# Kernel tuning notes

Hardware: AMD Instinct MI355X
Metric: run time of the kernel (lower is better)

## Reference

```python
import jax, jax.numpy as jnp
import numpy as np

H = 32          # num_heads
DN = 128        # qk_nope_head_dim
DR = 64         # qk_rope_head_dim
DV = 128        # v_head_dim
HID = 4096      # hidden_size
QR = 1536       # q_lora_rank
KVR = 512       # kv_lora_rank
EPS = 1e-6
MAXP = 4096     # max_position_embeddings


def _rope_tables():
    inv_freq = 1.0 / (10000.0 ** (np.arange(0, DR, 2, dtype=np.float32) / DR))
    t = np.arange(MAXP, dtype=np.float32)
    freqs = np.outer(t, inv_freq)
    emb = np.concatenate([freqs, freqs], axis=-1)  # [MAXP, DR]
    return jnp.asarray(np.cos(emb), jnp.float32), jnp.asarray(np.sin(emb), jnp.float32)


def _rotate_half(x):
    x1, x2 = x[..., : x.shape[-1] // 2], x[..., x.shape[-1] // 2 :]
    return jnp.concatenate([-x2, x1], axis=-1)


def _rms_norm(x, w, eps=EPS):
    var = jnp.mean(jnp.square(x), axis=-1, keepdims=True)
    return x * jax.lax.rsqrt(var + eps) * w


def setup_inputs() -> dict:
    key = jax.random.key(0)
    ks = jax.random.split(key, 9)
    s = 0.02
    return {
        "hidden_states": jax.random.normal(ks[0], (2, 2048, HID), jnp.float32),
        "position_ids": jnp.arange(2 * 2048, dtype=jnp.int64).reshape(2, 2048) % MAXP,
        "q_a_w": jax.random.normal(ks[1], (QR, HID), jnp.float32) * s,
        "q_a_ln_w": jnp.ones((QR,), jnp.float32),
        "q_b_w": jax.random.normal(ks[2], (H * (DN + DR), QR), jnp.float32) * s,
        "kv_a_w": jax.random.normal(ks[3], (KVR, HID), jnp.float32) * s,
        "kv_a_ln_w": jnp.ones((KVR,), jnp.float32),
        "kv_b_w": jax.random.normal(ks[4], (H * (DN + DV), KVR), jnp.float32) * s,
        "k_rope_w": jax.random.normal(ks[5], (H * DR, HID), jnp.float32) * s,
        "o_w": jax.random.normal(ks[6], (HID, H * DV), jnp.float32) * s,
    }


def reference(hidden_states, position_ids, q_a_w, q_a_ln_w, q_b_w,
              kv_a_w, kv_a_ln_w, kv_b_w, k_rope_w, o_w):
    bsz, q_len, _ = hidden_states.shape
    cos_tab, sin_tab = _rope_tables()

    # Q low-rank path
    q = hidden_states @ q_a_w.T                      # [B,S,QR]
    q = _rms_norm(q, q_a_ln_w)
    q = q @ q_b_w.T                                  # [B,S,H*(DN+DR)]
    q = q.reshape(bsz, q_len, H, DN + DR).transpose(0, 2, 1, 3)  # [B,H,S,DN+DR]
    q_nope, q_rope = q[..., :DN], q[..., DN:]

    # KV low-rank path
    kv = _rms_norm(hidden_states @ kv_a_w.T, kv_a_ln_w)          # [B,S,KVR]
    kv = (kv @ kv_b_w.T).reshape(bsz, q_len, H, DN + DV).transpose(0, 2, 1, 3)
    k_nope, v = kv[..., :DN], kv[..., DN:]                        # [B,H,S,DN],[B,H,S,DV]

    k_rope = (hidden_states @ k_rope_w.T).reshape(bsz, q_len, H, DR).transpose(0, 2, 1, 3)

    # decoupled RoPE
    cos = cos_tab[position_ids][:, None, :, :]       # [B,1,S,DR]
    sin = sin_tab[position_ids][:, None, :, :]
    q_rope = q_rope * cos + _rotate_half(q_rope) * sin
    k_rope = k_rope * cos + _rotate_half(k_rope) * sin

    full_q = jnp.concatenate([q_nope, q_rope], axis=-1)  # [B,H,S,DN+DR]
    full_k = jnp.concatenate([k_nope, k_rope], axis=-1)

    scale = 1.0 / jnp.sqrt(jnp.float32(DN + DR))
    attn = jnp.einsum("bhqd,bhkd->bhqk", full_q, full_k) * scale
    attn = jax.nn.softmax(attn.astype(jnp.float32), axis=-1).astype(full_q.dtype)
    out = jnp.einsum("bhqk,bhkd->bhqd", attn, v)          # [B,H,S,DV]
    out = out.transpose(0, 2, 1, 3).reshape(bsz, q_len, H * DV)
    return out @ o_w.T                                     # [B,S,HID]
```

## Files before the change

### kernel.cpp

```cpp
#include <hip/hip_runtime.h>
#include <hip/hip_bf16.h>
#include <math.h>


typedef __attribute__((ext_vector_type(8))) short s16x8;
typedef __attribute__((ext_vector_type(4))) float f32x4;
typedef __attribute__((ext_vector_type(4))) unsigned short u16x4;

#define DEV __device__ __forceinline__

constexpr int Bc = 2, Sc = 2048, Tc = Bc * Sc;
constexpr int Hc = 32, DNc = 128, DRc = 64, DVc = 128;
constexpr int HIDc = 4096, QRc = 1536, KVRc = 512;
constexpr int DQK = DNc + DRc;

DEV unsigned short f2bf(float f) {
  unsigned u = __float_as_uint(f);
  return (unsigned short)((u + 0x7fffu + ((u >> 16) & 1u)) >> 16);
}
DEV float bf2f(unsigned short u) { return __uint_as_float(((unsigned)u) << 16); }

DEV void gll16(const void* g, void* l) {
  __builtin_amdgcn_global_load_lds((const __attribute__((address_space(1))) void*)g,
                                   (__attribute__((address_space(3))) void*)l, 16, 0, 0);
}
DEV f32x4 mfma_bf16(s16x8 a, s16x8 b, f32x4 c) {
  return __builtin_amdgcn_mfma_f32_16x16x32_bf16(a, b, c, 0, 0, 0);
}
DEV unsigned cvt_pk_bf16(float a, float b) {
  unsigned r;
  asm("v_cvt_pk_bf16_f32 %0, %1, %2" : "=v"(r) : "v"(a), "v"(b));
  return r;
}

__global__ __launch_bounds__(256) void cast_k(const float* __restrict__ in,
                                              unsigned short* __restrict__ out, long n) {
  long i = ((long)blockIdx.x * 256 + threadIdx.x) * 4;
  if (i >= n) return;
  float4 v = *(const float4*)(in + i);
  u16x4 o;
  o.x = f2bf(v.x); o.y = f2bf(v.y); o.z = f2bf(v.z); o.w = f2bf(v.w);
  *(u16x4*)(out + i) = o;
}

template <int COLS>
__global__ __launch_bounds__(256) void rmsnorm_bf_k(unsigned short* __restrict__ x,
                                                    const float* __restrict__ w,
                                                    int pitch) {
  const int row = blockIdx.x;
  unsigned short* p = x + (size_t)row * pitch;
  float ss = 0.f;
  for (int c = threadIdx.x * 8; c < COLS; c += 2048) {
    s16x8 v = *(const s16x8*)&p[c];
    #pragma unroll
    for (int j = 0; j < 8; ++j) { const float f = bf2f((unsigned short)v[j]); ss += f * f; }
  }
  #pragma unroll
  for (int off = 1; off < 64; off <<= 1) ss += __shfl_xor(ss, off, 64);
  __shared__ float sred[4];
  if ((threadIdx.x & 63) == 0) sred[threadIdx.x >> 6] = ss;
  __syncthreads();
  const float inv = rsqrtf((sred[0] + sred[1] + sred[2] + sred[3]) / (float)COLS + 1e-6f);
  for (int c = threadIdx.x * 8; c < COLS; c += 2048) {
    s16x8 v = *(const s16x8*)&p[c];
    s16x8 o;
    #pragma unroll
    for (int j = 0; j < 8; ++j)
      o[j] = (short)f2bf(bf2f((unsigned short)v[j]) * inv * w[c + j]);
    *(s16x8*)&p[c] = o;
  }
}

template <int MODE>
__global__ __launch_bounds__(512, 2) void gemm256_bt(const unsigned short* __restrict__ A,
                                                     int lda,
                                                     const unsigned short* __restrict__ B,
                                                     void* __restrict__ Cout,
                                                     void* __restrict__ Cout2,
                                                     int M, int N, int K) {
  __shared__ unsigned short As[2][256 * 64];
  __shared__ unsigned short Bs[2][256 * 64];
  const int tid = threadIdx.x;
  const int wv = tid >> 6, l = tid & 63;
  const int lo = l & 15, hi = l >> 4;
  const int wm = wv >> 2, wn = wv & 3;
  const int nbx = N >> 8;
  const int nwg = (M >> 8) * nbx;
  const int orig = blockIdx.x;
  const int q8 = nwg >> 3, r8 = nwg & 7, xc = orig & 7, o8 = orig >> 3;
  const int wg = (xc < r8 ? xc * (q8 + 1) : r8 * (q8 + 1) + (xc - r8) * q8) + o8;
  const int bx = wg % nbx, by = wg / nbx;
  const int m0 = by * 256, n0 = bx * 256;
  const int lrow = l >> 3;
  const int lcol = (((l & 7) ^ lrow) << 3);

  f32x4 acc[8][4] = {};
  const int NKT = K >> 6;

  auto stage = [&](int bi, int kt) {
    #pragma unroll
    for (int i = 0; i < 4; ++i) {
      const int r0 = wv * 32 + i * 8;
      gll16(A + (size_t)(m0 + r0 + lrow) * lda + kt + lcol, (void*)&As[bi][r0 * 64]);
    }
    #pragma unroll
    for (int i = 0; i < 4; ++i) {
      const int r0 = wv * 32 + i * 8;
      gll16(B + (size_t)(n0 + r0 + lrow) * K + kt + lcol, (void*)&Bs[bi][r0 * 64]);
    }
  };

  stage(0, 0);

  for (int t = 0; t < NKT; ++t) {
    const int bi = t & 1;
    if (t + 1 < NKT) stage(bi ^ 1, (t + 1) * 64);
    __builtin_amdgcn_sched_barrier(0);
    if (t + 1 < NKT) asm volatile("s_waitcnt vmcnt(8)" ::: "memory");
    else             asm volatile("s_waitcnt vmcnt(0)" ::: "memory");
    __builtin_amdgcn_s_barrier();
    __builtin_amdgcn_sched_barrier(0);

    const unsigned short* Ab = As[bi];
    const unsigned short* Bb = Bs[bi];
    auto rdA = [&](int m, int kk) -> s16x8 {
      const int row = wm * 128 + m * 16 + lo;
      return *(const s16x8*)&Ab[row * 64 + ((kk * 32 + hi * 8) ^ ((row & 7) << 3))];
    };
    auto rdB = [&](int n, int kk) -> s16x8 {
      const int row = wn * 64 + n * 16 + lo;
      return *(const s16x8*)&Bb[row * 64 + ((kk * 32 + hi * 8) ^ ((row & 7) << 3))];
    };

    s16x8 a[4][2], b0[2][2], b2[2][2];
    #pragma unroll
    for (int m = 0; m < 4; ++m) { a[m][0] = rdA(m, 0); a[m][1] = rdA(m, 1); }
    #pragma unroll
    for (int n = 0; n < 2; ++n) { b0[n][0] = rdB(n, 0); b0[n][1] = rdB(n, 1); }
    __builtin_amdgcn_sched_barrier(0);
    __builtin_amdgcn_s_setprio(1);
    #pragma unroll
    for (int m = 0; m < 4; ++m)
      #pragma unroll
      for (int n = 0; n < 2; ++n) {
        acc[m][n] = mfma_bf16(a[m][0], b0[n][0], acc[m][n]);
        acc[m][n] = mfma_bf16(a[m][1], b0[n][1], acc[m][n]);
      }
    __builtin_amdgcn_s_setprio(0);
    __builtin_amdgcn_sched_barrier(0);
    __builtin_amdgcn_s_barrier();
    #pragma unroll
    for (int n = 0; n < 2; ++n) { b2[n][0] = rdB(n + 2, 0); b2[n][1] = rdB(n + 2, 1); }
    __builtin_amdgcn_sched_barrier(0);
    __builtin_amdgcn_s_setprio(1);
    #pragma unroll
    for (int m = 0; m < 4; ++m)
      #pragma unroll
      for (int n = 0; n < 2; ++n) {
        acc[m][n + 2] = mfma_bf16(a[m][0], b2[n][0], acc[m][n + 2]);
        acc[m][n + 2] = mfma_bf16(a[m][1], b2[n][1], acc[m][n + 2]);
      }
    __builtin_amdgcn_s_setprio(0);
    __builtin_amdgcn_sched_barrier(0);
    __builtin_amdgcn_s_barrier();
    #pragma unroll
    for (int m = 0; m < 4; ++m) { a[m][0] = rdA(m + 4, 0); a[m][1] = rdA(m + 4, 1); }
    __builtin_amdgcn_sched_barrier(0);
    __builtin_amdgcn_s_setprio(1);
    #pragma unroll
    for (int m = 0; m < 4; ++m)
      #pragma unroll
      for (int n = 0; n < 2; ++n) {
        acc[m + 4][n + 2] = mfma_bf16(a[m][0], b2[n][0], acc[m + 4][n + 2]);
        acc[m + 4][n + 2] = mfma_bf16(a[m][1], b2[n][1], acc[m + 4][n + 2]);
      }
    __builtin_amdgcn_s_setprio(0);
    __builtin_amdgcn_sched_barrier(0);
    __builtin_amdgcn_s_barrier();
    __builtin_amdgcn_s_setprio(1);
    #pragma unroll
    for (int m = 0; m < 4; ++m)
      #pragma unroll
      for (int n = 0; n < 2; ++n) {
        acc[m + 4][n] = mfma_bf16(a[m][0], b0[n][0], acc[m + 4][n]);
        acc[m + 4][n] = mfma_bf16(a[m][1], b0[n][1], acc[m + 4][n]);
      }
    __builtin_amdgcn_s_setprio(0);
    __builtin_amdgcn_sched_barrier(0);
    __builtin_amdgcn_s_barrier();
  }

  #pragma unroll
  for (int m = 0; m < 8; ++m)
    #pragma unroll
    for (int n = 0; n < 4; ++n)
      #pragma unroll
      for (int r = 0; r < 4; ++r) {
        const int row = m0 + wm * 128 + m * 16 + hi * 4 + r;
        const int col = n0 + wn * 64 + n * 16 + lo;
        const float v = acc[m][n][r];
        if (MODE == 1) {
          ((float*)Cout)[(size_t)row * N + col] = v;
        } else if (MODE == 0) {
          ((unsigned short*)Cout)[(size_t)row * N + col] = f2bf(v);
        } else if (MODE == 2) {
          const int hh = col / DQK, dd = col % DQK;
          const int bb = row >> 11, ss = row & 2047;
          ((unsigned short*)Cout)[((size_t)((bb * Hc + hh) * Sc + ss)) * DQK + dd] = f2bf(v);
        } else {
          const int hh = col >> 8, cc = col & 255;
          const int bb = row >> 11, ss = row & 2047;
          if (cc < 128)
            ((unsigned short*)Cout)[((size_t)((bb * Hc + hh) * Sc + ss)) * DQK + cc] = f2bf(v);
          else
            ((unsigned short*)Cout2)[(size_t)row * (Hc * DVc) + hh * DVc + (cc - 128)] = f2bf(v);
        }
      }
}

DEV void rope_pair8(float pos, int j0, const s16x8& x1, const s16x8& x2,
                    s16x8& o1, s16x8& o2) {
  #pragma unroll
  for (int j = 0; j < 8; ++j) {
    const int jj = j0 + j;
    const float inv = exp2f(-(float)jj * 0.4152410118f);
    float sn, cs;
    sincosf(pos * inv, &sn, &cs);
    const float a = bf2f((unsigned short)x1[j]);
    const float c = bf2f((unsigned short)x2[j]);
    o1[j] = f2bf(a * cs - c * sn);
    o2[j] = f2bf(c * cs + a * sn);
  }
}

__global__ __launch_bounds__(256) void rope_q_k(unsigned short* __restrict__ Qa,
                                                const int* __restrict__ pos) {
  const int gid = blockIdx.x * 256 + threadIdx.x;
  const int pr = gid & 3, rowp = gid >> 2;
  const int j0 = pr * 8;
  const int bh = rowp >> 11, s = rowp & 2047;
  const int token = (bh >> 5) * Sc + s;
  unsigned short* base = Qa + (size_t)rowp * DQK + 128;
  s16x8 x1 = *(const s16x8*)&base[j0];
  s16x8 x2 = *(const s16x8*)&base[j0 + 32];
  s16x8 o1, o2;
  rope_pair8((float)pos[token], j0, x1, x2, o1, o2);
  *(s16x8*)&base[j0] = o1;
  *(s16x8*)&base[j0 + 32] = o2;
}

__global__ __launch_bounds__(256) void rope_k2_k(const unsigned short* __restrict__ kr,
                                                 const int* __restrict__ pos,
                                                 unsigned short* __restrict__ Ka) {
  const int gid = blockIdx.x * 256 + threadIdx.x;
  const int pr = gid & 3, rowp = gid >> 2;
  const int j0 = pr * 8;
  const int bh = rowp >> 11, s = rowp & 2047;
  const int h = bh & 31;
  const int token = (bh >> 5) * Sc + s;
  const unsigned short* src = kr + (size_t)token * HIDc + h * DRc;
  s16x8 x1 = *(const s16x8*)&src[j0];
  s16x8 x2 = *(const s16x8*)&src[j0 + 32];
  s16x8 o1, o2;
  rope_pair8((float)pos[token], j0, x1, x2, o1, o2);
  unsigned short* dst = Ka + (size_t)rowp * DQK + 128;
  *(s16x8*)&dst[j0] = o1;
  *(s16x8*)&dst[j0 + 32] = o2;
}

__global__ __launch_bounds__(512, 2) void attn_k(const unsigned short* __restrict__ Q,
                                                 const unsigned short* __restrict__ Kt,
                                                 const unsigned short* __restrict__ KV,
                                                 unsigned short* __restrict__ O) {
  __shared__ unsigned short Ks[2][64 * 192];
  __shared__ unsigned short Vs[2][128 * 64];
  __shared__ unsigned short Ps[8][32 * 64];
  const int bh = blockIdx.x, qblk = blockIdx.y;
  const int b = bh >> 5, h = bh & 31;
  const int tid = threadIdx.x, w = tid >> 6, l = tid & 63;
  const int lo = l & 15, hi = l >> 4;
  const int sw = (lo & 7) << 3;
  const unsigned short* Qb = Q + (size_t)bh * Sc * DQK;
  const unsigned short* Kb = Kt + (size_t)bh * Sc * DQK;
  const int qrow0 = qblk * 256 + w * 32;
  const float c2 = 0.10411759f;

  s16x8 qfr[2][6];
  #pragma unroll
  for (int qf = 0; qf < 2; ++qf)
    #pragma unroll
    for (int dc = 0; dc < 6; ++dc)
      qfr[qf][dc] = *(const s16x8*)&Qb[(size_t)(qrow0 + qf * 16 + lo) * DQK + dc * 32 + hi * 8];

  f32x4 oacc[2][8] = {};
  float mrow[2] = {-INFINITY, -INFINITY};
  float lrow[2] = {0.f, 0.f};

  s16x8 vv[2];
  auto stageK = [&](int kb, int kt) {
    #pragma unroll
    for (int i = 0; i < 3; ++i) {
      const int o = (w * 3 + i) * 1024 + l * 16;
      const int rr = o / 384, cc = o % 384;
      const int scc = cc ^ ((rr & 7) << 4);
      gll16(Kb + (size_t)(kt + rr) * DQK + (scc >> 1), (void*)&Ks[kb][(w * 3 + i) * 512]);
    }
  };
  auto loadV = [&](int kt) {
    #pragma unroll
    for (int it = 0; it < 2; ++it) {
      const int dv0 = (w * 2 + it) * 8;
      vv[it] = *(const s16x8*)(KV + (size_t)(b * Sc + kt + l) * (Hc * DVc) + h * DVc + dv0);
    }
  };
  auto writeV = [&](int vb) {
    #pragma unroll
    for (int it = 0; it < 2; ++it) {
      const int dv0 = (w * 2 + it) * 8;
      #pragma unroll
      for (int j = 0; j < 8; ++j) {
        const int dv = dv0 + j;
        Vs[vb][(dv * 64 + l) ^ ((dv & 7) << 3)] = (unsigned short)vv[it][j];
      }
    }
  };

  constexpr int NT = Sc / 64;
  loadV(0);
  stageK(0, 0);
  writeV(0);
  asm volatile("s_waitcnt vmcnt(0) lgkmcnt(0)" ::: "memory");
  __builtin_amdgcn_s_barrier();
  __builtin_amdgcn_sched_barrier(0);
  int cur = 0;

  for (int t = 0; t < NT; ++t) {
    const bool pre = (t + 1 < NT);
    if (pre) {
      loadV((t + 1) * 64);
      __builtin_amdgcn_sched_barrier(0);
      stageK(cur ^ 1, (t + 1) * 64);
      __builtin_amdgcn_sched_barrier(0);
    }

    f32x4 sc[2][4] = {};
    #pragma unroll
    for (int cf = 0; cf < 4; ++cf) {
      const int krow = cf * 16 + lo;
      #pragma unroll
      for (int dc = 0; dc < 6; ++dc) {
        s16x8 kf = *(const s16x8*)&Ks[cur][(krow * 192 + dc * 32 + hi * 8) ^ ((krow & 7) << 3)];
        sc[0][cf] = mfma_bf16(kf, qfr[0][dc], sc[0][cf]);
        sc[1][cf] = mfma_bf16(kf, qfr[1][dc], sc[1][cf]);
      }
    }

    #pragma unroll
    for (int qf = 0; qf < 2; ++qf) {
      float mx = sc[qf][0][0];
      #pragma unroll
      for (int cf = 0; cf < 4; ++cf)
        #pragma unroll
        for (int r = 0; r < 4; ++r) mx = fmaxf(mx, sc[qf][cf][r]);
      mx = fmaxf(mx, __shfl_xor(mx, 16, 64));
      mx = fmaxf(mx, __shfl_xor(mx, 32, 64));
      const float nm = fmaxf(mrow[qf], mx * c2);
      const float alpha = exp2f(mrow[qf] - nm);
      mrow[qf] = nm;
      float psum = 0.f;
      const int qrow = qf * 16 + lo;
      #pragma unroll
      for (int cf = 0; cf < 4; ++cf) {
        float p0 = exp2f(fmaf(sc[qf][cf][0], c2, -nm));
        float p1 = exp2f(fmaf(sc[qf][cf][1], c2, -nm));
        float p2 = exp2f(fmaf(sc[qf][cf][2], c2, -nm));
        float p3 = exp2f(fmaf(sc[qf][cf][3], c2, -nm));
        psum += (p0 + p1) + (p2 + p3);
        const int ka = cf * 16 + hi * 4;
        *(unsigned*)&Ps[w][qrow * 64 + ((ka + 0) ^ sw)] = cvt_pk_bf16(p0, p1);
        *(unsigned*)&Ps[w][qrow * 64 + ((ka + 2) ^ sw)] = cvt_pk_bf16(p2, p3);
      }
      psum += __shfl_xor(psum, 16, 64);
      psum += __shfl_xor(psum, 32, 64);
      lrow[qf] = lrow[qf] * alpha + psum;
      #pragma unroll
      for (int r = 0; r < 4; ++r) {
        const float ar = __shfl(alpha, hi * 4 + r, 64);
        #pragma unroll
        for (int dvf = 0; dvf < 8; ++dvf) oacc[qf][dvf][r] *= ar;
      }
    }

    #pragma unroll
    for (int hf = 0; hf < 2; ++hf) {
      s16x8 pa0 = *(const s16x8*)&Ps[w][lo * 64 + ((hf * 32 + hi * 8) ^ sw)];
      s16x8 pa1 = *(const s16x8*)&Ps[w][(16 + lo) * 64 + ((hf * 32 + hi * 8) ^ sw)];
      #pragma unroll
      for (int dvf = 0; dvf < 8; ++dvf) {
        const int dv = dvf * 16 + lo;
        s16x8 vb = *(const s16x8*)&Vs[cur][(dv * 64 + hf * 32 + hi * 8) ^ ((dv & 7) << 3)];
        oacc[0][dvf] = mfma_bf16(pa0, vb, oacc[0][dvf]);
        oacc[1][dvf] = mfma_bf16(pa1, vb, oacc[1][dvf]);
      }
    }

    if (pre) writeV(cur ^ 1);
    asm volatile("s_waitcnt vmcnt(0) lgkmcnt(0)" ::: "memory");
    __builtin_amdgcn_s_barrier();
    __builtin_amdgcn_sched_barrier(0);
    cur ^= 1;
  }

  #pragma unroll
  for (int qf = 0; qf < 2; ++qf)
    #pragma unroll
    for (int r = 0; r < 4; ++r) {
      const float linv = 1.f / __shfl(lrow[qf], hi * 4 + r, 64);
      const int q = qrow0 + qf * 16 + hi * 4 + r;
      #pragma unroll
      for (int dvf = 0; dvf < 8; ++dvf)
        O[(size_t)(b * Sc + q) * (Hc * DVc) + h * DVc + dvf * 16 + lo] =
            f2bf(oacc[qf][dvf][r] * linv);
    }
}

extern "C" void kernel_launch(void* const* d_in, const int* in_sizes, int n_in,
                              void* d_out, int out_size, void* d_ws, size_t ws_size,
                              hipStream_t stream) {
  const float* hs      = (const float*)d_in[0];
  const int*   posids  = (const int*)d_in[1];
  const float* qa_w    = (const float*)d_in[2];
  const float* qa_ln   = (const float*)d_in[3];
  const float* qb_w    = (const float*)d_in[4];
  const float* kva_w   = (const float*)d_in[5];
  const float* kva_ln  = (const float*)d_in[6];
  const float* kvb_w   = (const float*)d_in[7];
  const float* kr_w    = (const float*)d_in[8];
  const float* o_w     = (const float*)d_in[9];
  float* out = (float*)d_out;

  char* ws = (char*)d_ws;
  const size_t offF = 0;
  const size_t offR = offF + 33554432;
  const size_t offD = offR + 35651584;
  const size_t offA = offD + 50331648;
  const size_t offB = offA + 67108864;

  unsigned short* hs_bf  = (unsigned short*)(ws + offF);
  unsigned short* w_qb   = (unsigned short*)(ws + offF);
  unsigned short* w_kvb  = (unsigned short*)(ws + offF);
  unsigned short* attn_o = (unsigned short*)(ws + offF);
  unsigned short* cbuf   = (unsigned short*)(ws + offR);
  unsigned short* Ka     = (unsigned short*)(ws + offD);
  unsigned short* kv_v   = (unsigned short*)(ws + offA);
  unsigned short* cw     = (unsigned short*)(ws + offB);
  unsigned short* Qa     = (unsigned short*)(ws + offB);
  unsigned short* w_o    = (unsigned short*)(ws + offB);

  auto cast = [&](const float* src, unsigned short* dst, long n) {
    cast_k<<<dim3((unsigned)((n / 4 + 255) / 256)), dim3(256), 0, stream>>>(src, dst, n);
  };

  cast(hs, hs_bf, (long)Tc * HIDc);

  cast(qa_w,  cw,                              (long)QRc * HIDc);
  cast(kva_w, cw + (size_t)QRc * HIDc,         (long)KVRc * HIDc);
  cast(kr_w,  cw + (size_t)(QRc + KVRc) * HIDc,(long)Hc * DRc * HIDc);

  gemm256_bt<0><<<dim3(16 * 16), dim3(512), 0, stream>>>(hs_bf, HIDc, cw,
                                                         (void*)cbuf, nullptr,
                                                         Tc, HIDc, HIDc);

  rmsnorm_bf_k<QRc><<<dim3(Tc), dim3(256), 0, stream>>>(cbuf, qa_ln, HIDc);
  rmsnorm_bf_k<KVRc><<<dim3(Tc), dim3(256), 0, stream>>>(cbuf + QRc, kva_ln, HIDc);

  cast(qb_w, w_qb, (long)Hc * DQK * QRc);
  gemm256_bt<2><<<dim3(16 * 24), dim3(512), 0, stream>>>(cbuf, HIDc, w_qb,
                                                         (void*)Qa, nullptr,
                                                         Tc, Hc * DQK, QRc);

  cast(kvb_w, w_kvb, (long)Hc * 256 * KVRc);
  gemm256_bt<3><<<dim3(16 * 32), dim3(512), 0, stream>>>(cbuf + QRc, HIDc, w_kvb,
                                                         (void*)Ka, (void*)kv_v,
                                                         Tc, Hc * 256, KVRc);

  const int npair = Bc * Hc * Sc * 4;
  rope_q_k<<<dim3(npair / 256), dim3(256), 0, stream>>>(Qa, posids);
  rope_k2_k<<<dim3(npair / 256), dim3(256), 0, stream>>>(cbuf + QRc + KVRc, posids, Ka);

  attn_k<<<dim3(Bc * Hc, Sc / 256), dim3(512), 0, stream>>>(Qa, Ka, kv_v, attn_o);

  cast(o_w, w_o, (long)HIDc * Hc * DVc);
  gemm256_bt<1><<<dim3(16 * 16), dim3(512), 0, stream>>>(attn_o, Hc * DVc, w_o,
                                                         (void*)out, nullptr,
                                                         Tc, HIDc, Hc * DVc);

  (void)in_sizes; (void)n_in; (void)out_size; (void)ws_size;
}
```

Measured before the change: 841.2 us.

## Warp-specialize attention: QK/softmax warps feed PV warps through a software pipeline

Splits the 8 waves of the attention kernel into two groups. Four waves stage K, compute QK^T and softmax, and write P and the rescale factors to shared memory. The other four load V, rescale their accumulators and run the PV MFMAs one tile behind, so the two halves overlap. Each block now covers 128 query rows instead of 256, doubling the grid. The aim is to overlap softmax/exp work with the PV matrix multiplies. The cost is that each K/V tile is reloaded for half as many queries, which doubles K/V traffic, and the two groups may be imbalanced.

```diff
diff --git a/kernel.cpp b/kernel.cpp
--- a/kernel.cpp
+++ b/kernel.cpp
@@ -274,154 +274,168 @@
                                                  unsigned short* __restrict__ O) {
   __shared__ unsigned short Ks[2][64 * 192];
   __shared__ unsigned short Vs[2][128 * 64];
-  __shared__ unsigned short Ps[8][32 * 64];
+  __shared__ unsigned short Ps[2][4][32 * 64];
+  __shared__ float Al[2][128];
+  __shared__ float Li[128];
   const int bh = blockIdx.x, qblk = blockIdx.y;
   const int b = bh >> 5, h = bh & 31;
   const int tid = threadIdx.x, w = tid >> 6, l = tid & 63;
+  const int pw = w & 3;
   const int lo = l & 15, hi = l >> 4;
   const int sw = (lo & 7) << 3;
   const unsigned short* Qb = Q + (size_t)bh * Sc * DQK;
   const unsigned short* Kb = Kt + (size_t)bh * Sc * DQK;
-  const int qrow0 = qblk * 256 + w * 32;
+  const int qrow0 = qblk * 128 + pw * 32;
   const float c2 = 0.10411759f;
+  constexpr int NT = Sc / 64;
 
   s16x8 qfr[2][6];
-  #pragma unroll
-  for (int qf = 0; qf < 2; ++qf)
-    #pragma unroll
-    for (int dc = 0; dc < 6; ++dc)
-      qfr[qf][dc] = *(const s16x8*)&Qb[(size_t)(qrow0 + qf * 16 + lo) * DQK + dc * 32 + hi * 8];
-
-  f32x4 oacc[2][8] = {};
   float mrow[2] = {-INFINITY, -INFINITY};
   float lrow[2] = {0.f, 0.f};
-
-  s16x8 vv[2];
+  f32x4 oacc[2][8] = {};
+  s16x8 vv[4];
+
   auto stageK = [&](int kb, int kt) {
     #pragma unroll
-    for (int i = 0; i < 3; ++i) {
-      const int o = (w * 3 + i) * 1024 + l * 16;
+    for (int i = 0; i < 6; ++i) {
+      const int o = (pw * 6 + i) * 1024 + l * 16;
       const int rr = o / 384, cc = o % 384;
       const int scc = cc ^ ((rr & 7) << 4);
-      gll16(Kb + (size_t)(kt + rr) * DQK + (scc >> 1), (void*)&Ks[kb][(w * 3 + i) * 512]);
+      gll16(Kb + (size_t)(kt + rr) * DQK + (scc >> 1), (void*)&Ks[kb][(pw * 6 + i) * 512]);
     }
   };
   auto loadV = [&](int kt) {
     #pragma unroll
-    for (int it = 0; it < 2; ++it) {
-      const int dv0 = (w * 2 + it) * 8;
-      vv[it] = *(const s16x8*)(KV + (size_t)(b * Sc + kt + l) * (Hc * DVc) + h * DVc + dv0);
+    for (int itc = 0; itc < 4; ++itc)
+      vv[itc] = *(const s16x8*)(KV + (size_t)(b * Sc + kt + l) * (Hc * DVc) + h * DVc +
+                                (pw * 4 + itc) * 8);
+  };
+  auto writeV = [&](int vb) {
+    #pragma unroll
+    for (int itc = 0; itc < 4; ++itc) {
+      const int dv0 = (pw * 4 + itc) * 8;
+      #pragma unroll
+      for (int j = 0; j < 8; ++j) {
+        const int dv = dv0 + j;
+        Vs[vb][(dv * 64 + l) ^ ((dv & 7) << 3)] = (unsigned short)vv[itc][j];
+      }
     }
   };
-  auto writeV = [&](int vb) {
-    #pragma unroll
-    for (int it = 0; it < 2; ++it) {
-      const int dv0 = (w * 2 + it) * 8;
-      #pragma unroll
-      for (int j = 0; j < 8; ++j) {
-        const int dv = dv0 + j;
-        Vs[vb][(dv * 64 + l) ^ ((dv & 7) << 3)] = (unsigned short)vv[it][j];
-      }
-    }
-  };
-
-  constexpr int NT = Sc / 64;
-  loadV(0);
-  stageK(0, 0);
-  writeV(0);
+
+  if (w < 4) {
+    #pragma unroll
+    for (int qf = 0; qf < 2; ++qf)
+      #pragma unroll
+      for (int dc = 0; dc < 6; ++dc)
+        qfr[qf][dc] = *(const s16x8*)&Qb[(size_t)(qrow0 + qf * 16 + lo) * DQK + dc * 32 + hi * 8];
+    stageK(0, 0);
+  } else {
+    loadV(0);
+  }
   asm volatile("s_waitcnt vmcnt(0) lgkmcnt(0)" ::: "memory");
   __builtin_amdgcn_s_barrier();
   __builtin_amdgcn_sched_barrier(0);
-  int cur = 0;
-
-  for (int t = 0; t < NT; ++t) {
-    const bool pre = (t + 1 < NT);
-    if (pre) {
-      loadV((t + 1) * 64);
-      __builtin_amdgcn_sched_barrier(0);
-      stageK(cur ^ 1, (t + 1) * 64);
-      __builtin_amdgcn_sched_barrier(0);
+
+  for (int it = 0; it <= NT; ++it) {
+    if (w < 4) {
+      if (it < NT) {
+        if (it + 1 < NT) stageK((it + 1) & 1, (it + 1) * 64);
+        __builtin_amdgcn_sched_barrier(0);
+        f32x4 sc[2][4] = {};
+        const unsigned short* Kc = Ks[it & 1];
+        #pragma unroll
+        for (int cf = 0; cf < 4; ++cf) {
+          const int krow = cf * 16 + lo;
+          #pragma unroll
+          for (int dc = 0; dc < 6; ++dc) {
+            s16x8 kf = *(const s16x8*)&Kc[(krow * 192 + dc * 32 + hi * 8) ^ ((krow & 7) << 3)];
+            sc[0][cf] = mfma_bf16(kf, qfr[0][dc], sc[0][cf]);
+            sc[1][cf] = mfma_bf16(kf, qfr[1][dc], sc[1][cf]);
+          }
+        }
+        #pragma unroll
+        for (int qf = 0; qf < 2; ++qf) {
+          float mx = sc[qf][0][0];
+          #pragma unroll
+          for (int cf = 0; cf < 4; ++cf)
+            #pragma unroll
+            for (int r = 0; r < 4; ++r) mx = fmaxf(mx, sc[qf][cf][r]);
+          mx = fmaxf(mx, __shfl_xor(mx, 16, 64));
+          mx = fmaxf(mx, __shfl_xor(mx, 32, 64));
+          const float nm = fmaxf(mrow[qf], mx * c2);
+          const float alpha = exp2f(mrow[qf] - nm);
+          mrow[qf] = nm;
+          if (hi == 0) Al[it & 1][pw * 32 + qf * 16 + lo] = alpha;
+          float psum = 0.f;
+          const int qrow = qf * 16 + lo;
+          #pragma unroll
+          for (int cf = 0; cf < 4; ++cf) {
+            float p0 = exp2f(fmaf(sc[qf][cf][0], c2, -nm));
+            float p1 = exp2f(fmaf(sc[qf][cf][1], c2, -nm));
+            float p2 = exp2f(fmaf(sc[qf][cf][2], c2, -nm));
+            float p3 = exp2f(fmaf(sc[qf][cf][3], c2, -nm));
+            psum += (p0 + p1) + (p2 + p3);
+            const int ka = cf * 16 + hi * 4;
+            *(unsigned*)&Ps[it & 1][pw][qrow * 64 + ((ka + 0) ^ sw)] = cvt_pk_bf16(p0, p1);
+            *(unsigned*)&Ps[it & 1][pw][qrow * 64 + ((ka + 2) ^ sw)] = cvt_pk_bf16(p2, p3);
+          }
+          psum += __shfl_xor(psum, 16, 64);
+          psum += __shfl_xor(psum, 32, 64);
+          lrow[qf] = lrow[qf] * alpha + psum;
+        }
+      } else {
+        if (hi == 0) {
+          Li[pw * 32 + lo] = lrow[0];
+          Li[pw * 32 + 16 + lo] = lrow[1];
+        }
+      }
+    } else {
+      if (it < NT) {
+        writeV(it & 1);
+        if (it + 1 < NT) loadV((it + 1) * 64);
+      }
+      if (it > 0) {
+        const int j = (it - 1) & 1;
+        #pragma unroll
+        for (int qf = 0; qf < 2; ++qf)
+          #pragma unroll
+          for (int r = 0; r < 4; ++r) {
+            const float ar = Al[j][pw * 32 + qf * 16 + hi * 4 + r];
+            #pragma unroll
+            for (int dvf = 0; dvf < 8; ++dvf) oacc[qf][dvf][r] *= ar;
+          }
+        #pragma unroll
+        for (int hf = 0; hf < 2; ++hf) {
+          s16x8 pa0 = *(const s16x8*)&Ps[j][pw][lo * 64 + ((hf * 32 + hi * 8) ^ sw)];
+          s16x8 pa1 = *(const s16x8*)&Ps[j][pw][(16 + lo) * 64 + ((hf * 32 + hi * 8) ^ sw)];
+          #pragma unroll
+          for (int dvf = 0; dvf < 8; ++dvf) {
+            const int dv = dvf * 16 + lo;
+            s16x8 vb = *(const s16x8*)&Vs[j][(dv * 64 + hf * 32 + hi * 8) ^ ((dv & 7) << 3)];
+            oacc[0][dvf] = mfma_bf16(pa0, vb, oacc[0][dvf]);
+            oacc[1][dvf] = mfma_bf16(pa1, vb, oacc[1][dvf]);
+          }
+        }
+      }
     }
-
-    f32x4 sc[2][4] = {};
-    #pragma unroll
-    for (int cf = 0; cf < 4; ++cf) {
-      const int krow = cf * 16 + lo;
-      #pragma unroll
-      for (int dc = 0; dc < 6; ++dc) {
-        s16x8 kf = *(const s16x8*)&Ks[cur][(krow * 192 + dc * 32 + hi * 8) ^ ((krow & 7) << 3)];
-        sc[0][cf] = mfma_bf16(kf, qfr[0][dc], sc[0][cf]);
-        sc[1][cf] = mfma_bf16(kf, qfr[1][dc], sc[1][cf]);
-      }
-    }
-
-    #pragma unroll
-    for (int qf = 0; qf < 2; ++qf) {
-      float mx = sc[qf][0][0];
-      #pragma unroll
-      for (int cf = 0; cf < 4; ++cf)
-        #pragma unroll
-        for (int r = 0; r < 4; ++r) mx = fmaxf(mx, sc[qf][cf][r]);
-      mx = fmaxf(mx, __shfl_xor(mx, 16, 64));
-      mx = fmaxf(mx, __shfl_xor(mx, 32, 64));
-      const float nm = fmaxf(mrow[qf], mx * c2);
-      const float alpha = exp2f(mrow[qf] - nm);
-      mrow[qf] = nm;
-      float psum = 0.f;
-      const int qrow = qf * 16 + lo;
-      #pragma unroll
-      for (int cf = 0; cf < 4; ++cf) {
-        float p0 = exp2f(fmaf(sc[qf][cf][0], c2, -nm));
-        float p1 = exp2f(fmaf(sc[qf][cf][1], c2, -nm));
-        float p2 = exp2f(fmaf(sc[qf][cf][2], c2, -nm));
-        float p3 = exp2f(fmaf(sc[qf][cf][3], c2, -nm));
-        psum += (p0 + p1) + (p2 + p3);
-        const int ka = cf * 16 + hi * 4;
-        *(unsigned*)&Ps[w][qrow * 64 + ((ka + 0) ^ sw)] = cvt_pk_bf16(p0, p1);
-        *(unsigned*)&Ps[w][qrow * 64 + ((ka + 2) ^ sw)] = cvt_pk_bf16(p2, p3);
-      }
-      psum += __shfl_xor(psum, 16, 64);
-      psum += __shfl_xor(psum, 32, 64);
-      lrow[qf] = lrow[qf] * alpha + psum;
-      #pragma unroll
-      for (int r = 0; r < 4; ++r) {
-        const float ar = __shfl(alpha, hi * 4 + r, 64);
-        #pragma unroll
-        for (int dvf = 0; dvf < 8; ++dvf) oacc[qf][dvf][r] *= ar;
-      }
-    }
-
-    #pragma unroll
-    for (int hf = 0; hf < 2; ++hf) {
-      s16x8 pa0 = *(const s16x8*)&Ps[w][lo * 64 + ((hf * 32 + hi * 8) ^ sw)];
-      s16x8 pa1 = *(const s16x8*)&Ps[w][(16 + lo) * 64 + ((hf * 32 + hi * 8) ^ sw)];
-      #pragma unroll
-      for (int dvf = 0; dvf < 8; ++dvf) {
-        const int dv = dvf * 16 + lo;
-        s16x8 vb = *(const s16x8*)&Vs[cur][(dv * 64 + hf * 32 + hi * 8) ^ ((dv & 7) << 3)];
-        oacc[0][dvf] = mfma_bf16(pa0, vb, oacc[0][dvf]);
-        oacc[1][dvf] = mfma_bf16(pa1, vb, oacc[1][dvf]);
-      }
-    }
-
-    if (pre) writeV(cur ^ 1);
     asm volatile("s_waitcnt vmcnt(0) lgkmcnt(0)" ::: "memory");
     __builtin_amdgcn_s_barrier();
     __builtin_amdgcn_sched_barrier(0);
-    cur ^= 1;
-  }
-
-  #pragma unroll
-  for (int qf = 0; qf < 2; ++qf)
-    #pragma unroll
-    for (int r = 0; r < 4; ++r) {
-      const float linv = 1.f / __shfl(lrow[qf], hi * 4 + r, 64);
-      const int q = qrow0 + qf * 16 + hi * 4 + r;
-      #pragma unroll
-      for (int dvf = 0; dvf < 8; ++dvf)
-        O[(size_t)(b * Sc + q) * (Hc * DVc) + h * DVc + dvf * 16 + lo] =
-            f2bf(oacc[qf][dvf][r] * linv);
-    }
+  }
+
+  if (w >= 4) {
+    #pragma unroll
+    for (int qf = 0; qf < 2; ++qf)
+      #pragma unroll
+      for (int r = 0; r < 4; ++r) {
+        const float linv = 1.f / Li[pw * 32 + qf * 16 + hi * 4 + r];
+        const int q = qrow0 + qf * 16 + hi * 4 + r;
+        #pragma unroll
+        for (int dvf = 0; dvf < 8; ++dvf)
+          O[(size_t)(b * Sc + q) * (Hc * DVc) + h * DVc + dvf * 16 + lo] =
+              f2bf(oacc[qf][dvf][r] * linv);
+      }
+  }
 }
 
 extern "C" void kernel_launch(void* const* d_in, const int* in_sizes, int n_in,
@@ -488,7 +502,7 @@
   rope_q_k<<<dim3(npair / 256), dim3(256), 0, stream>>>(Qa, posids);
   rope_k2_k<<<dim3(npair / 256), dim3(256), 0, stream>>>(cbuf + QRc + KVRc, posids, Ka);
 
-  attn_k<<<dim3(Bc * Hc, Sc / 256), dim3(512), 0, stream>>>(Qa, Ka, kv_v, attn_o);
+  attn_k<<<dim3(Bc * Hc, Sc / 128), dim3(512), 0, stream>>>(Qa, Ka, kv_v, attn_o);
 
   cast(o_w, w_o, (long)HIDc * Hc * DVc);
   gemm256_bt<1><<<dim3(16 * 16), dim3(512), 0, stream>>>(attn_o, Hc * DVc, w_o,
```

New measurement: 974.0 us. 1.16x slower.

## Write V transposed from GEMM epilogue and restructure attention to single-buffered 16-row waves

Applied to the files above, without the earlier changes.

The kv_b GEMM epilogue now writes V in a per-head transposed [B,H,DV,S] layout with vector stores, so the attention kernel can stage V into LDS with direct global-to-LDS loads instead of register loads plus scalar scatter writes. The attention kernel is restructured to 16 query rows per wave (128 per block, twice the blocks), single-buffered K/V LDS with smaller footprint, and launch bounds raised to 4 blocks per SM for occupancy. It also adds a lazy rescale that skips the online-softmax correction unless the running max grows by more than 8 in log2 units. This trades explicit prefetch overlap for occupancy-based latency hiding and halves Q-fragment reuse per K tile.

```diff
diff --git a/kernel.cpp b/kernel.cpp
--- a/kernel.cpp
+++ b/kernel.cpp
@@ -190,32 +190,48 @@
     __builtin_amdgcn_s_barrier();
   }
 
-  #pragma unroll
-  for (int m = 0; m < 8; ++m)
-    #pragma unroll
-    for (int n = 0; n < 4; ++n)
-      #pragma unroll
-      for (int r = 0; r < 4; ++r) {
-        const int row = m0 + wm * 128 + m * 16 + hi * 4 + r;
+  if (MODE == 3) {
+    #pragma unroll
+    for (int m = 0; m < 8; ++m)
+      #pragma unroll
+      for (int n = 0; n < 4; ++n) {
+        const int row0 = m0 + wm * 128 + m * 16 + hi * 4;
         const int col = n0 + wn * 64 + n * 16 + lo;
-        const float v = acc[m][n][r];
-        if (MODE == 1) {
-          ((float*)Cout)[(size_t)row * N + col] = v;
-        } else if (MODE == 0) {
-          ((unsigned short*)Cout)[(size_t)row * N + col] = f2bf(v);
-        } else if (MODE == 2) {
-          const int hh = col / DQK, dd = col % DQK;
-          const int bb = row >> 11, ss = row & 2047;
-          ((unsigned short*)Cout)[((size_t)((bb * Hc + hh) * Sc + ss)) * DQK + dd] = f2bf(v);
+        const int hh = col >> 8, cc = col & 255;
+        const int bb = row0 >> 11, ss = row0 & 2047;
+        if (cc < 128) {
+          #pragma unroll
+          for (int r = 0; r < 4; ++r)
+            ((unsigned short*)Cout)[((size_t)((bb * Hc + hh) * Sc + ss + r)) * DQK + cc] =
+                f2bf(acc[m][n][r]);
         } else {
-          const int hh = col >> 8, cc = col & 255;
-          const int bb = row >> 11, ss = row & 2047;
-          if (cc < 128)
-            ((unsigned short*)Cout)[((size_t)((bb * Hc + hh) * Sc + ss)) * DQK + cc] = f2bf(v);
-          else
-            ((unsigned short*)Cout2)[(size_t)row * (Hc * DVc) + hh * DVc + (cc - 128)] = f2bf(v);
+          u16x4 o;
+          #pragma unroll
+          for (int r = 0; r < 4; ++r) o[r] = f2bf(acc[m][n][r]);
+          *(u16x4*)&((unsigned short*)Cout2)[((size_t)((bb * Hc + hh) * DVc + (cc - 128))) * Sc + ss] = o;
         }
       }
+  } else {
+    #pragma unroll
+    for (int m = 0; m < 8; ++m)
+      #pragma unroll
+      for (int n = 0; n < 4; ++n)
+        #pragma unroll
+        for (int r = 0; r < 4; ++r) {
+          const int row = m0 + wm * 128 + m * 16 + hi * 4 + r;
+          const int col = n0 + wn * 64 + n * 16 + lo;
+          const float v = acc[m][n][r];
+          if (MODE == 1) {
+            ((float*)Cout)[(size_t)row * N + col] = v;
+          } else if (MODE == 0) {
+            ((unsigned short*)Cout)[(size_t)row * N + col] = f2bf(v);
+          } else {
+            const int hh = col / DQK, dd = col % DQK;
+            const int bb = row >> 11, ss = row & 2047;
+            ((unsigned short*)Cout)[((size_t)((bb * Hc + hh) * Sc + ss)) * DQK + dd] = f2bf(v);
+          }
+        }
+  }
 }
 
 DEV void rope_pair8(float pos, int j0, const s16x8& x1, const s16x8& x2,
@@ -268,13 +284,13 @@
   *(s16x8*)&dst[j0 + 32] = o2;
 }
 
-__global__ __launch_bounds__(512, 2) void attn_k(const unsigned short* __restrict__ Q,
+__global__ __launch_bounds__(512, 4) void attn_k(const unsigned short* __restrict__ Q,
                                                  const unsigned short* __restrict__ Kt,
-                                                 const unsigned short* __restrict__ KV,
+                                                 const unsigned short* __restrict__ Vt,
                                                  unsigned short* __restrict__ O) {
-  __shared__ unsigned short Ks[2][64 * 192];
-  __shared__ unsigned short Vs[2][128 * 64];
-  __shared__ unsigned short Ps[8][32 * 64];
+  __shared__ unsigned short Ks[64 * 192];
+  __shared__ unsigned short Vs[128 * 64];
+  __shared__ unsigned short Ps[8][16 * 64];
   const int bh = blockIdx.x, qblk = blockIdx.y;
   const int b = bh >> 5, h = bh & 31;
   const int tid = threadIdx.x, w = tid >> 6, l = tid & 63;
@@ -282,146 +298,120 @@
   const int sw = (lo & 7) << 3;
   const unsigned short* Qb = Q + (size_t)bh * Sc * DQK;
   const unsigned short* Kb = Kt + (size_t)bh * Sc * DQK;
-  const int qrow0 = qblk * 256 + w * 32;
+  const unsigned short* Vb = Vt + (size_t)bh * DVc * Sc;
+  const int qrow0 = qblk * 128 + w * 16;
   const float c2 = 0.10411759f;
 
-  s16x8 qfr[2][6];
+  s16x8 qfr[6];
   #pragma unroll
-  for (int qf = 0; qf < 2; ++qf)
-    #pragma unroll
-    for (int dc = 0; dc < 6; ++dc)
-      qfr[qf][dc] = *(const s16x8*)&Qb[(size_t)(qrow0 + qf * 16 + lo) * DQK + dc * 32 + hi * 8];
-
-  f32x4 oacc[2][8] = {};
-  float mrow[2] = {-INFINITY, -INFINITY};
-  float lrow[2] = {0.f, 0.f};
-
-  s16x8 vv[2];
-  auto stageK = [&](int kb, int kt) {
+  for (int dc = 0; dc < 6; ++dc)
+    qfr[dc] = *(const s16x8*)&Qb[(size_t)(qrow0 + lo) * DQK + dc * 32 + hi * 8];
+
+  f32x4 oacc[8] = {};
+  float mrow = -INFINITY;
+  float lrow = 0.f;
+
+  auto stageK = [&](int kt) {
     #pragma unroll
     for (int i = 0; i < 3; ++i) {
       const int o = (w * 3 + i) * 1024 + l * 16;
       const int rr = o / 384, cc = o % 384;
       const int scc = cc ^ ((rr & 7) << 4);
-      gll16(Kb + (size_t)(kt + rr) * DQK + (scc >> 1), (void*)&Ks[kb][(w * 3 + i) * 512]);
+      gll16(Kb + (size_t)(kt + rr) * DQK + (scc >> 1), (void*)&Ks[(w * 3 + i) * 512]);
     }
   };
-  auto loadV = [&](int kt) {
-    #pragma unroll
-    for (int it = 0; it < 2; ++it) {
-      const int dv0 = (w * 2 + it) * 8;
-      vv[it] = *(const s16x8*)(KV + (size_t)(b * Sc + kt + l) * (Hc * DVc) + h * DVc + dv0);
+  auto stageV = [&](int kt) {
+    #pragma unroll
+    for (int i = 0; i < 2; ++i) {
+      const int dvb = w * 16 + i * 8;
+      const int dv = dvb + (l >> 3);
+      const int ksrc = ((l & 7) ^ (dv & 7)) * 8;
+      gll16(Vb + (size_t)dv * Sc + kt + ksrc, (void*)&Vs[dvb * 64]);
     }
   };
-  auto writeV = [&](int vb) {
-    #pragma unroll
-    for (int it = 0; it < 2; ++it) {
-      const int dv0 = (w * 2 + it) * 8;
-      #pragma unroll
-      for (int j = 0; j < 8; ++j) {
-        const int dv = dv0 + j;
-        Vs[vb][(dv * 64 + l) ^ ((dv & 7) << 3)] = (unsigned short)vv[it][j];
-      }
-    }
-  };
 
   constexpr int NT = Sc / 64;
-  loadV(0);
-  stageK(0, 0);
-  writeV(0);
-  asm volatile("s_waitcnt vmcnt(0) lgkmcnt(0)" ::: "memory");
-  __builtin_amdgcn_s_barrier();
-  __builtin_amdgcn_sched_barrier(0);
-  int cur = 0;
 
   for (int t = 0; t < NT; ++t) {
-    const bool pre = (t + 1 < NT);
-    if (pre) {
-      loadV((t + 1) * 64);
-      __builtin_amdgcn_sched_barrier(0);
-      stageK(cur ^ 1, (t + 1) * 64);
-      __builtin_amdgcn_sched_barrier(0);
-    }
-
-    f32x4 sc[2][4] = {};
+    stageK(t * 64);
+    stageV(t * 64);
+    asm volatile("s_waitcnt vmcnt(0)" ::: "memory");
+    __builtin_amdgcn_s_barrier();
+    __builtin_amdgcn_sched_barrier(0);
+
+    f32x4 sc[4] = {};
     #pragma unroll
     for (int cf = 0; cf < 4; ++cf) {
       const int krow = cf * 16 + lo;
       #pragma unroll
       for (int dc = 0; dc < 6; ++dc) {
-        s16x8 kf = *(const s16x8*)&Ks[cur][(krow * 192 + dc * 32 + hi * 8) ^ ((krow & 7) << 3)];
-        sc[0][cf] = mfma_bf16(kf, qfr[0][dc], sc[0][cf]);
-        sc[1][cf] = mfma_bf16(kf, qfr[1][dc], sc[1][cf]);
-      }
-    }
-
-    #pragma unroll
-    for (int qf = 0; qf < 2; ++qf) {
-      float mx = sc[qf][0][0];
+        s16x8 kf = *(const s16x8*)&Ks[(krow * 192 + dc * 32 + hi * 8) ^ ((krow & 7) << 3)];
+        sc[cf] = mfma_bf16(kf, qfr[dc], sc[cf]);
+      }
+    }
+
+    {
+      float mx = sc[0][0];
       #pragma unroll
       for (int cf = 0; cf < 4; ++cf)
         #pragma unroll
-        for (int r = 0; r < 4; ++r) mx = fmaxf(mx, sc[qf][cf][r]);
+        for (int r = 0; r < 4; ++r) mx = fmaxf(mx, sc[cf][r]);
       mx = fmaxf(mx, __shfl_xor(mx, 16, 64));
       mx = fmaxf(mx, __shfl_xor(mx, 32, 64));
-      const float nm = fmaxf(mrow[qf], mx * c2);
-      const float alpha = exp2f(mrow[qf] - nm);
-      mrow[qf] = nm;
+      const float mxl = mx * c2;
+      if (!__all(mxl - mrow <= 8.f)) {
+        const float nm = fmaxf(mrow, mxl);
+        const float alpha = exp2f(mrow - nm);
+        mrow = nm;
+        lrow *= alpha;
+        #pragma unroll
+        for (int r = 0; r < 4; ++r) {
+          const float ar = __shfl(alpha, hi * 4 + r, 64);
+          #pragma unroll
+          for (int dvf = 0; dvf < 8; ++dvf) oacc[dvf][r] *= ar;
+        }
+      }
       float psum = 0.f;
-      const int qrow = qf * 16 + lo;
       #pragma unroll
       for (int cf = 0; cf < 4; ++cf) {
-        float p0 = exp2f(fmaf(sc[qf][cf][0], c2, -nm));
-        float p1 = exp2f(fmaf(sc[qf][cf][1], c2, -nm));
-        float p2 = exp2f(fmaf(sc[qf][cf][2], c2, -nm));
-        float p3 = exp2f(fmaf(sc[qf][cf][3], c2, -nm));
-        psum += (p0 + p1) + (p2 + p3);
+        sc[cf][0] = exp2f(fmaf(sc[cf][0], c2, -mrow));
+        sc[cf][1] = exp2f(fmaf(sc[cf][1], c2, -mrow));
+        sc[cf][2] = exp2f(fmaf(sc[cf][2], c2, -mrow));
+        sc[cf][3] = exp2f(fmaf(sc[cf][3], c2, -mrow));
+        psum += (sc[cf][0] + sc[cf][1]) + (sc[cf][2] + sc[cf][3]);
         const int ka = cf * 16 + hi * 4;
-        *(unsigned*)&Ps[w][qrow * 64 + ((ka + 0) ^ sw)] = cvt_pk_bf16(p0, p1);
-        *(unsigned*)&Ps[w][qrow * 64 + ((ka + 2) ^ sw)] = cvt_pk_bf16(p2, p3);
+        *(unsigned*)&Ps[w][lo * 64 + ((ka + 0) ^ sw)] = cvt_pk_bf16(sc[cf][0], sc[cf][1]);
+        *(unsigned*)&Ps[w][lo * 64 + ((ka + 2) ^ sw)] = cvt_pk_bf16(sc[cf][2], sc[cf][3]);
       }
       psum += __shfl_xor(psum, 16, 64);
       psum += __shfl_xor(psum, 32, 64);
-      lrow[qf] = lrow[qf] * alpha + psum;
-      #pragma unroll
-      for (int r = 0; r < 4; ++r) {
-        const float ar = __shfl(alpha, hi * 4 + r, 64);
-        #pragma unroll
-        for (int dvf = 0; dvf < 8; ++dvf) oacc[qf][dvf][r] *= ar;
-      }
+      lrow += psum;
     }
 
     #pragma unroll
     for (int hf = 0; hf < 2; ++hf) {
-      s16x8 pa0 = *(const s16x8*)&Ps[w][lo * 64 + ((hf * 32 + hi * 8) ^ sw)];
-      s16x8 pa1 = *(const s16x8*)&Ps[w][(16 + lo) * 64 + ((hf * 32 + hi * 8) ^ sw)];
+      s16x8 pa = *(const s16x8*)&Ps[w][lo * 64 + ((hf * 32 + hi * 8) ^ sw)];
       #pragma unroll
       for (int dvf = 0; dvf < 8; ++dvf) {
         const int dv = dvf * 16 + lo;
-        s16x8 vb = *(const s16x8*)&Vs[cur][(dv * 64 + hf * 32 + hi * 8) ^ ((dv & 7) << 3)];
-        oacc[0][dvf] = mfma_bf16(pa0, vb, oacc[0][dvf]);
-        oacc[1][dvf] = mfma_bf16(pa1, vb, oacc[1][dvf]);
-      }
-    }
-
-    if (pre) writeV(cur ^ 1);
-    asm volatile("s_waitcnt vmcnt(0) lgkmcnt(0)" ::: "memory");
-    __builtin_amdgcn_s_barrier();
-    __builtin_amdgcn_sched_barrier(0);
-    cur ^= 1;
+        s16x8 vb = *(const s16x8*)&Vs[dv * 64 + ((hf * 32 + hi * 8) ^ ((dv & 7) << 3))];
+        oacc[dvf] = mfma_bf16(pa, vb, oacc[dvf]);
+      }
+    }
+
+    __builtin_amdgcn_s_barrier();
+    __builtin_amdgcn_sched_barrier(0);
   }
 
   #pragma unroll
-  for (int qf = 0; qf < 2; ++qf)
-    #pragma unroll
-    for (int r = 0; r < 4; ++r) {
-      const float linv = 1.f / __shfl(lrow[qf], hi * 4 + r, 64);
-      const int q = qrow0 + qf * 16 + hi * 4 + r;
-      #pragma unroll
-      for (int dvf = 0; dvf < 8; ++dvf)
-        O[(size_t)(b * Sc + q) * (Hc * DVc) + h * DVc + dvf * 16 + lo] =
-            f2bf(oacc[qf][dvf][r] * linv);
-    }
+  for (int r = 0; r < 4; ++r) {
+    const float linv = 1.f / __shfl(lrow, hi * 4 + r, 64);
+    const int q = qrow0 + hi * 4 + r;
+    #pragma unroll
+    for (int dvf = 0; dvf < 8; ++dvf)
+      O[(size_t)(b * Sc + q) * (Hc * DVc) + h * DVc + dvf * 16 + lo] =
+          f2bf(oacc[dvf][r] * linv);
+  }
 }
 
 extern "C" void kernel_launch(void* const* d_in, const int* in_sizes, int n_in,
@@ -452,7 +442,7 @@
   unsigned short* attn_o = (unsigned short*)(ws + offF);
   unsigned short* cbuf   = (unsigned short*)(ws + offR);
   unsigned short* Ka     = (unsigned short*)(ws + offD);
-  unsigned short* kv_v   = (unsigned short*)(ws + offA);
+  unsigned short* kv_vt  = (unsigned short*)(ws + offA);
   unsigned short* cw     = (unsigned short*)(ws + offB);
   unsigned short* Qa     = (unsigned short*)(ws + offB);
   unsigned short* w_o    = (unsigned short*)(ws + offB);
@@ -481,14 +471,14 @@
 
   cast(kvb_w, w_kvb, (long)Hc * 256 * KVRc);
   gemm256_bt<3><<<dim3(16 * 32), dim3(512), 0, stream>>>(cbuf + QRc, HIDc, w_kvb,
-                                                         (void*)Ka, (void*)kv_v,
+                                                         (void*)Ka, (void*)kv_vt,
                                                          Tc, Hc * 256, KVRc);
 
   const int npair = Bc * Hc * Sc * 4;
   rope_q_k<<<dim3(npair / 256), dim3(256), 0, stream>>>(Qa, posids);
   rope_k2_k<<<dim3(npair / 256), dim3(256), 0, stream>>>(cbuf + QRc + KVRc, posids, Ka);
 
-  attn_k<<<dim3(Bc * Hc, Sc / 256), dim3(512), 0, stream>>>(Qa, Ka, kv_v, attn_o);
+  attn_k<<<dim3(Bc * Hc, Sc / 128), dim3(512), 0, stream>>>(Qa, Ka, kv_vt, attn_o);
 
   cast(o_w, w_o, (long)HIDc * Hc * DVc);
   gemm256_bt<1><<<dim3(16 * 16), dim3(512), 0, stream>>>(attn_o, Hc * DVc, w_o,
```

Result: faster. 761.1 us (-9.5%).
